# Optimization experiments

Measured on AMD Instinct MI355X. Metric: run time of the kernel, lower is better.

## Reference

```python
import jax, jax.numpy as jnp
import numpy as np

# dims: B batch, S seq, IN input, H lstm hidden, OUT output, N memory_size, W memory_width
B, S, IN, H, OUT, N, W = 128, 32, 512, 1024, 512, 16384, 128
C = OUT + W + (2 * W + 3)  # controller_output_size = 899


def setup_inputs() -> dict:
    key = jax.random.key(0)
    ks = jax.random.split(key, 16)
    def p(k, shape, s=0.02):
        return jax.random.normal(k, shape, jnp.float32) * s
    return {
        'x': jax.random.normal(ks[0], (B, S, IN), jnp.float32),
        'memory': p(ks[1], (N, W), 0.1),
        'Wih': p(ks[2], (4 * H, IN + W)), 'Whh': p(ks[3], (4 * H, H)),
        'bih': jnp.zeros(4 * H, jnp.float32), 'bhh': jnp.zeros(4 * H, jnp.float32),
        'Wout': p(ks[4], (C, H)), 'bout': jnp.zeros(C, jnp.float32),
        'rkW': p(ks[5], (W, C)), 'rkb': jnp.zeros(W, jnp.float32),
        'rbW': p(ks[6], (1, C)), 'rbb': jnp.zeros(1, jnp.float32),
        'rgW': p(ks[7], (1, C)), 'rgb': jnp.zeros(1, jnp.float32),
        'wkW': p(ks[8], (W, C)), 'wkb': jnp.zeros(W, jnp.float32),
        'wbW': p(ks[9], (1, C)), 'wbb': jnp.zeros(1, jnp.float32),
        'wgW': p(ks[10], (1, C)), 'wgb': jnp.zeros(1, jnp.float32),
        'erW': p(ks[11], (W, C)), 'erb': jnp.zeros(W, jnp.float32),
        'adW': p(ks[12], (W, C)), 'adb': jnp.zeros(W, jnp.float32),
        'pW': p(ks[13], (OUT, OUT)), 'pb': jnp.zeros(OUT, jnp.float32),
    }


def _l2norm(v, axis):
    n = jnp.linalg.norm(v, axis=axis, keepdims=True)
    return v / jnp.maximum(n, 1e-12)


def reference(x, memory, Wih, Whh, bih, bhh, Wout, bout,
              rkW, rkb, rbW, rbb, rgW, rgb,
              wkW, wkb, wbW, wbb, wgW, wgb,
              erW, erb, adW, adb, pW, pb):
    Bq, Sq, _ = x.shape
    Nq, Wq = memory.shape
    Hq = Whh.shape[1]
    out_size = pW.shape[0]
    sp = jax.nn.softplus
    uniform = jnp.full((Bq, Nq), 1.0 / Nq, x.dtype)

    def addressing(keyv, beta, gamma, prev_w, mem):
        # cosine similarity -> softmax(beta*sim) -> interpolation with prev weights
        sim = _l2norm(keyv, 1) @ _l2norm(mem, 1).T        # [B, N]
        w = jax.nn.softmax(beta * sim, axis=1)
        return gamma * w + (1 - gamma) * prev_w

    def step(carry, xt):
        mem, h, c, prev_rw, prev_rv = carry
        ci = jnp.concatenate([xt, prev_rv], axis=1)       # [B, IN+W]
        g = ci @ Wih.T + h @ Whh.T + bih + bhh
        i_, f_, gg, o_ = jnp.split(g, 4, axis=1)          # torch LSTM gate order i,f,g,o
        c = jax.nn.sigmoid(f_) * c + jax.nn.sigmoid(i_) * jnp.tanh(gg)
        h = jax.nn.sigmoid(o_) * jnp.tanh(c)
        co = h @ Wout.T + bout                            # controller output [B, C]
        # read head
        rkey = co @ rkW.T + rkb
        rbeta = sp(co @ rbW.T + rbb)
        rgamma = 1 + sp(co @ rgW.T + rgb)
        rw = addressing(rkey, rbeta, rgamma, prev_rw, mem)
        # write head (prev weights = uniform, per source)
        wkey = co @ wkW.T + wkb
        wbeta = sp(co @ wbW.T + wbb)
        wgamma = 1 + sp(co @ wgW.T + wgb)
        ww = addressing(wkey, wbeta, wgamma, uniform, mem)
        er = jax.nn.sigmoid(co @ erW.T + erb)             # [B, W]
        ad = jnp.tanh(co @ adW.T + adb)                   # [B, W]
        # MemoryBank.write sums erase/add terms over batch (shared global memory)
        erase = jnp.einsum('bn,bw->nw', ww, er)
        addt = jnp.einsum('bn,bw->nw', ww, ad)
        mem = mem * (1 - erase) + addt
        rv = rw @ mem                                     # read after write [B, W]
        out = co[:, :out_size] @ pW.T + pb
        return (mem, h, c, rw, rv), out

    init = (memory,
            jnp.zeros((Bq, Hq), x.dtype), jnp.zeros((Bq, Hq), x.dtype),
            uniform, jnp.zeros((Bq, Wq), x.dtype))
    _, outs = jax.lax.scan(step, init, jnp.swapaxes(x, 0, 1))
    return jnp.swapaxes(outs, 0, 1)                       # [B, S, OUT]
```

## Files before the change

### kernel.cpp

```cpp
#include <hip/hip_runtime.h>

typedef __attribute__((ext_vector_type(8))) short bf16x8;
typedef __attribute__((ext_vector_type(4))) float f32x4;

__device__ __forceinline__ float bf2f(unsigned short u) {
  union { float f; unsigned int i; } v; v.i = ((unsigned int)u) << 16; return v.f;
}
__device__ __forceinline__ unsigned short f2bf(float f) {
  union { float f; unsigned int i; } v; v.f = f;
  unsigned int r = v.i + 0x7fffu + ((v.i >> 16) & 1u);
  return (unsigned short)(r >> 16);
}
__device__ __forceinline__ float sigf(float x) { return 1.0f / (1.0f + expf(-x)); }
__device__ __forceinline__ float softplusf(float x) {
  return (x > 20.0f) ? x : log1pf(expf(x));
}
__device__ __forceinline__ float sat(float v) {
  return fminf(fmaxf(v, -1.0e6f), 1.0e6f);
}
__device__ __forceinline__ float ldx(const void* p, int is32, long i) {
  return is32 ? ((const float*)p)[i] : bf2f(((const unsigned short*)p)[i]);
}
template<int A32>
__device__ __forceinline__ bf16x8 load8(const void* base, long off) {
  if (A32) {
    const float* p = (const float*)base + off;
    f32x4 a = *(const f32x4*)p;
    f32x4 b = *(const f32x4*)(p + 4);
    bf16x8 r;
    r[0] = (short)f2bf(a[0]); r[1] = (short)f2bf(a[1]);
    r[2] = (short)f2bf(a[2]); r[3] = (short)f2bf(a[3]);
    r[4] = (short)f2bf(b[0]); r[5] = (short)f2bf(b[1]);
    r[6] = (short)f2bf(b[2]); r[7] = (short)f2bf(b[3]);
    return r;
  }
  return *(const bf16x8*)((const unsigned short*)base + off);
}


__global__ __launch_bounds__(64) void probe_dtype(
    const unsigned int* __restrict__ w, int* __restrict__ flags)
{
  const int lane = threadIdx.x;
  int cnt = 0;
  for (int i = 0; i < 16; ++i) {
    unsigned int word = w[lane * 16 + i];
    float av = fabsf(bf2f((unsigned short)(word & 0xFFFFu)));
    if (av > 1.0e-4f && av < 1.0f) cnt++;
  }
  #pragma unroll
  for (int off = 32; off > 0; off >>= 1) cnt += __shfl_xor(cnt, off);
  if (lane == 0) flags[1] = (cnt > 512) ? 0 : 1;
}

__global__ __launch_bounds__(64) void probe_layout(int* __restrict__ flags) {
  const int lane = threadIdx.x;
  const int qr = lane & 15, quad = lane >> 4;
  bf16x8 a, b;
  #pragma unroll
  for (int j = 0; j < 8; ++j) {
    int k = quad * 8 + j;
    a[j] = (short)f2bf((k == qr) ? 1.0f : 0.0f);
    b[j] = (short)f2bf((float)(k + 1));
  }
  f32x4 acc = {0.0f, 0.0f, 0.0f, 0.0f};
  acc = __builtin_amdgcn_mfma_f32_16x16x32_bf16(a, b, acc, 0, 0, 0);
  bool ok0 = true, ok1 = true;
  #pragma unroll
  for (int rg = 0; rg < 4; ++rg) {
    ok0 = ok0 && (acc[rg] == (float)(quad * 4 + rg + 1));
    ok1 = ok1 && (acc[rg] == (float)(qr + 1));
  }
  int a0 = __all(ok0 ? 1 : 0);
  int a1 = __all(ok1 ? 1 : 0);
  if (lane == 0) flags[0] = a0 ? 0 : (a1 ? 1 : 0);
}

template<int BM, int BN, int EPI, int A32, int BT>
__global__ __launch_bounds__(256) void gemm_pipe(
    const void* __restrict__ A, int lda,
    const unsigned short* __restrict__ B, int ldb,
    int kChunk, int Mtot, int Ntot,
    float* __restrict__ C, long long ldc, unsigned short* __restrict__ Cb,
    const int* __restrict__ flags)
{
  constexpr int LDT = 72;
  constexpr int AI = BM / 32;
  constexpr int BI = BN / 32;
  __shared__ unsigned short smem[2][(BM + BN) * LDT];
  const int tid = threadIdx.x;
  const int lane = tid & 63, wid = tid >> 6;
  const int wm = wid & 1, wn = wid >> 1;
  constexpr int WM = BM / 2, WN = BN / 2;
  constexpr int TM = WM / 16, TN = WN / 16;
  const int m0 = blockIdx.x * BM, n0 = blockIdx.y * BN;
  const int kBeg = blockIdx.z * kChunk;
  const int qr = lane & 15, quad = lane >> 4;
  const int NIT = kChunk >> 6;

  f32x4 acc[TM][TN] = {};
  bf16x8 ar[AI], br[BI];

  auto loadAB = [&](int k0) {
    #pragma unroll
    for (int i = 0; i < AI; ++i) {
      int lin = i * 256 + tid; int row = lin >> 3, q = (lin & 7) << 3;
      ar[i] = load8<A32>(A, (long)(m0 + row) * lda + k0 + q);
    }
    #pragma unroll
    for (int i = 0; i < BI; ++i) {
      int lin = i * 256 + tid;
      if (BT) {
        int kl = lin >> 3, nq = (lin & 7) << 3;
        br[i] = *(const bf16x8*)(B + (long)(k0 + kl) * ldb + n0 + nq);
      } else {
        int row = lin >> 3, q = (lin & 7) << 3;
        br[i] = *(const bf16x8*)(B + (long)(n0 + row) * ldb + k0 + q);
      }
    }
  };
  auto stage = [&](int buf) {
    #pragma unroll
    for (int i = 0; i < AI; ++i) {
      int lin = i * 256 + tid; int row = lin >> 3, q = (lin & 7) << 3;
      *(bf16x8*)&smem[buf][row * LDT + q] = ar[i];
    }
    #pragma unroll
    for (int i = 0; i < BI; ++i) {
      int lin = i * 256 + tid;
      if (BT) {
        int kl = lin >> 3, nq = (lin & 7) << 3;
        #pragma unroll
        for (int j = 0; j < 8; ++j)
          smem[buf][(BM + nq + j) * LDT + kl] = (unsigned short)br[i][j];
      } else {
        int row = lin >> 3, q = (lin & 7) << 3;
        *(bf16x8*)&smem[buf][(BM + row) * LDT + q] = br[i];
      }
    }
  };

  loadAB(kBeg);
  stage(0);
  __syncthreads();
  for (int it = 0; it < NIT; ++it) {
    if (it + 1 < NIT) loadAB(kBeg + (it + 1) * 64);
    const unsigned short* As = &smem[it & 1][0];
    const unsigned short* Bs = &smem[it & 1][BM * LDT];
    #pragma unroll
    for (int ks = 0; ks < 64; ks += 32) {
      bf16x8 af[TM], bfv[TN];
      #pragma unroll
      for (int mt = 0; mt < TM; ++mt)
        af[mt] = *(const bf16x8*)&As[(wm * WM + mt * 16 + qr) * LDT + ks + quad * 8];
      #pragma unroll
      for (int nt = 0; nt < TN; ++nt)
        bfv[nt] = *(const bf16x8*)&Bs[(wn * WN + nt * 16 + qr) * LDT + ks + quad * 8];
      #pragma unroll
      for (int mt = 0; mt < TM; ++mt)
        #pragma unroll
        for (int nt = 0; nt < TN; ++nt)
          acc[mt][nt] = __builtin_amdgcn_mfma_f32_16x16x32_bf16(af[mt], bfv[nt], acc[mt][nt], 0, 0, 0);
    }
    if (it + 1 < NIT) { stage((it + 1) & 1); __syncthreads(); }
  }

  const int swap = flags[0];
  #pragma unroll
  for (int mt = 0; mt < TM; ++mt)
    #pragma unroll
    for (int nt = 0; nt < TN; ++nt)
      #pragma unroll
      for (int rg = 0; rg < 4; ++rg) {
        int ri = swap ? qr : (quad * 4 + rg);
        int ci = swap ? (quad * 4 + rg) : qr;
        int gm = m0 + wm * WM + mt * 16 + ri;
        int gn = n0 + wn * WN + nt * 16 + ci;
        float v = sat(acc[mt][nt][rg]);
        if (EPI == 2) Cb[(size_t)gm * ldc + gn] = f2bf(v);
        else C[(size_t)blockIdx.z * Mtot * Ntot + (size_t)gm * Ntot + gn] = v;
      }
}

__global__ __launch_bounds__(256) void gemm_gates(
    const unsigned short* __restrict__ A, const unsigned short* __restrict__ B,
    const float* __restrict__ bsum2, float* __restrict__ c,
    unsigned short* __restrict__ nxt, const unsigned short* __restrict__ x_bf,
    int t, const int* __restrict__ flags)
{
  constexpr int LDT = 72;
  __shared__ unsigned short smem[2][128 * LDT];
  __shared__ float Ssc[64][65];
  const int tid = threadIdx.x;
  const int lane = tid & 63, wid = tid >> 6;
  const int wm = wid & 1, wn = wid >> 1;
  const int m0 = blockIdx.x * 64, n0 = blockIdx.y * 64;
  const int qr = lane & 15, quad = lane >> 4;
  const int NIT = 26;

  f32x4 acc[2][2] = {};
  bf16x8 ar[2], br[2];
  auto loadAB = [&](int k0) {
    #pragma unroll
    for (int i = 0; i < 2; ++i) {
      int lin = i * 256 + tid; int row = lin >> 3, q = (lin & 7) << 3;
      ar[i] = *(const bf16x8*)(A + (long)(m0 + row) * 1664 + k0 + q);
      br[i] = *(const bf16x8*)(B + (long)(n0 + row) * 1664 + k0 + q);
    }
  };
  auto stage = [&](int buf) {
    #pragma unroll
    for (int i = 0; i < 2; ++i) {
      int lin = i * 256 + tid; int row = lin >> 3, q = (lin & 7) << 3;
      *(bf16x8*)&smem[buf][row * LDT + q] = ar[i];
      *(bf16x8*)&smem[buf][(64 + row) * LDT + q] = br[i];
    }
  };
  loadAB(0); stage(0); __syncthreads();
  for (int it = 0; it < NIT; ++it) {
    if (it + 1 < NIT) loadAB((it + 1) * 64);
    const unsigned short* As = &smem[it & 1][0];
    const unsigned short* Bs = &smem[it & 1][64 * LDT];
    #pragma unroll
    for (int ks = 0; ks < 64; ks += 32) {
      bf16x8 af[2], bfv[2];
      #pragma unroll
      for (int mt = 0; mt < 2; ++mt)
        af[mt] = *(const bf16x8*)&As[(wm * 32 + mt * 16 + qr) * LDT + ks + quad * 8];
      #pragma unroll
      for (int nt = 0; nt < 2; ++nt)
        bfv[nt] = *(const bf16x8*)&Bs[(wn * 32 + nt * 16 + qr) * LDT + ks + quad * 8];
      #pragma unroll
      for (int mt = 0; mt < 2; ++mt)
        #pragma unroll
        for (int nt = 0; nt < 2; ++nt)
          acc[mt][nt] = __builtin_amdgcn_mfma_f32_16x16x32_bf16(af[mt], bfv[nt], acc[mt][nt], 0, 0, 0);
    }
    if (it + 1 < NIT) { stage((it + 1) & 1); __syncthreads(); }
  }

  const int swap = flags[0];
  #pragma unroll
  for (int mt = 0; mt < 2; ++mt)
    #pragma unroll
    for (int nt = 0; nt < 2; ++nt)
      #pragma unroll
      for (int rg = 0; rg < 4; ++rg) {
        int ri = swap ? qr : (quad * 4 + rg);
        int ci = swap ? (quad * 4 + rg) : qr;
        Ssc[wn * 32 + nt * 16 + ci][wm * 32 + mt * 16 + ri] = acc[mt][nt][rg];
      }
  __syncthreads();
  {
    const int jl = tid & 15, bh = tid >> 4;
    const int jg = (n0 >> 2) + jl;
    const float b0 = bsum2[n0 + jl * 4 + 0];
    const float b1 = bsum2[n0 + jl * 4 + 1];
    const float b2 = bsum2[n0 + jl * 4 + 2];
    const float b3 = bsum2[n0 + jl * 4 + 3];
    #pragma unroll
    for (int p = 0; p < 4; ++p) {
      int bl = bh + p * 16;
      int bb = m0 + bl;
      float gi_ = Ssc[jl * 4 + 0][bl] + b0;
      float gf  = Ssc[jl * 4 + 1][bl] + b1;
      float gg  = Ssc[jl * 4 + 2][bl] + b2;
      float go  = Ssc[jl * 4 + 3][bl] + b3;
      size_t cix = (size_t)bb * 1024 + jg;
      float cn = sat(sigf(gf) * c[cix] + sigf(gi_) * tanhf(gg));
      c[cix] = cn;
      nxt[bb * 1664 + 640 + jg] = f2bf(sigf(go) * tanhf(cn));
    }
  }
  if (t + 1 < 32) {
    int blk = blockIdx.y * 2 + blockIdx.x;
    #pragma unroll
    for (int i = 0; i < 2; ++i) {
      int e = blk * 512 + i * 256 + tid;
      nxt[(e >> 9) * 1664 + (e & 511)] = x_bf[(size_t)(t + 1) * 65536 + e];
    }
  }
}

__global__ __launch_bounds__(256) void gemm_heads(
    const unsigned short* __restrict__ Wcomb,
    const unsigned short* __restrict__ h, int ldb,
    const float* __restrict__ vcat,
    unsigned short* __restrict__ keys_n, unsigned short* __restrict__ EA,
    float* __restrict__ sc, void* __restrict__ outp, int t,
    const int* __restrict__ flags)
{
  constexpr int BM = 128, BN = 64, LDT = 72;
  __shared__ unsigned short smem[2][(BM + BN) * LDT];
  __shared__ float colss[64];
  __shared__ float cinv[64];
  const int tid = threadIdx.x;
  const int lane = tid & 63, wid = tid >> 6;
  const int wm = wid & 1, wn = wid >> 1;
  constexpr int TM = 4, TN = 2;
  const int m0 = blockIdx.x * BM, n0 = blockIdx.y * BN;
  const int qr = lane & 15, quad = lane >> 4;
  const int NIT = 16;

  f32x4 acc[TM][TN] = {};
  bf16x8 ar[4], br[2];
  auto loadAB = [&](int k0) {
    #pragma unroll
    for (int i = 0; i < 4; ++i) {
      int lin = i * 256 + tid; int row = lin >> 3, q = (lin & 7) << 3;
      ar[i] = *(const bf16x8*)(Wcomb + (long)(m0 + row) * 1024 + k0 + q);
    }
    #pragma unroll
    for (int i = 0; i < 2; ++i) {
      int lin = i * 256 + tid; int row = lin >> 3, q = (lin & 7) << 3;
      br[i] = *(const bf16x8*)(h + (long)(n0 + row) * ldb + k0 + q);
    }
  };
  auto stage = [&](int buf) {
    #pragma unroll
    for (int i = 0; i < 4; ++i) {
      int lin = i * 256 + tid; int row = lin >> 3, q = (lin & 7) << 3;
      *(bf16x8*)&smem[buf][row * LDT + q] = ar[i];
    }
    #pragma unroll
    for (int i = 0; i < 2; ++i) {
      int lin = i * 256 + tid; int row = lin >> 3, q = (lin & 7) << 3;
      *(bf16x8*)&smem[buf][(BM + row) * LDT + q] = br[i];
    }
  };

  loadAB(0);
  stage(0);
  __syncthreads();
  for (int it = 0; it < NIT; ++it) {
    if (it + 1 < NIT) loadAB((it + 1) * 64);
    const unsigned short* As = &smem[it & 1][0];
    const unsigned short* Bs = &smem[it & 1][BM * LDT];
    #pragma unroll
    for (int ks = 0; ks < 64; ks += 32) {
      bf16x8 af[TM], bfv[TN];
      #pragma unroll
      for (int mt = 0; mt < TM; ++mt)
        af[mt] = *(const bf16x8*)&smem[it & 1][(wm * 64 + mt * 16 + qr) * LDT + ks + quad * 8];
      #pragma unroll
      for (int nt = 0; nt < TN; ++nt)
        bfv[nt] = *(const bf16x8*)&Bs[(wn * 32 + nt * 16 + qr) * LDT + ks + quad * 8];
      (void)As;
      #pragma unroll
      for (int mt = 0; mt < TM; ++mt)
        #pragma unroll
        for (int nt = 0; nt < TN; ++nt)
          acc[mt][nt] = __builtin_amdgcn_mfma_f32_16x16x32_bf16(af[mt], bfv[nt], acc[mt][nt], 0, 0, 0);
    }
    if (it + 1 < NIT) { stage((it + 1) & 1); __syncthreads(); }
  }

  const int swap = flags[0];
  const int F = flags[1];
  #pragma unroll
  for (int mt = 0; mt < TM; ++mt)
    #pragma unroll
    for (int nt = 0; nt < TN; ++nt)
      #pragma unroll
      for (int rg = 0; rg < 4; ++rg) {
        int ri = swap ? qr : (quad * 4 + rg);
        int gm = m0 + wm * 64 + mt * 16 + ri;
        acc[mt][nt][rg] = sat(acc[mt][nt][rg] + vcat[gm]);
      }

  if (m0 < 256) {
    if (tid < 64) colss[tid] = 0.0f;
    __syncthreads();
    #pragma unroll
    for (int nt = 0; nt < TN; ++nt)
      #pragma unroll
      for (int rg = 0; rg < 4; ++rg) {
        float part = 0.0f;
        #pragma unroll
        for (int mt = 0; mt < TM; ++mt) {
          float v = acc[mt][nt][rg]; part += v * v;
        }
        int ci = swap ? (quad * 4 + rg) : qr;
        atomicAdd(&colss[wn * 32 + nt * 16 + ci], part);
      }
    __syncthreads();
    if (tid < 64) cinv[tid] = 1.0f / fmaxf(sqrtf(colss[tid]), 1e-12f);
    __syncthreads();
    const int head = m0 >> 7;
    #pragma unroll
    for (int mt = 0; mt < TM; ++mt)
      #pragma unroll
      for (int nt = 0; nt < TN; ++nt)
        #pragma unroll
        for (int rg = 0; rg < 4; ++rg) {
          int ri = swap ? qr : (quad * 4 + rg);
          int ci = swap ? (quad * 4 + rg) : qr;
          int w = wm * 64 + mt * 16 + ri;
          int cl = wn * 32 + nt * 16 + ci;
          keys_n[(size_t)(head * 128 + n0 + cl) * 128 + w] =
              f2bf(acc[mt][nt][rg] * cinv[cl]);
        }
  } else {
    #pragma unroll
    for (int mt = 0; mt < TM; ++mt)
      #pragma unroll
      for (int nt = 0; nt < TN; ++nt)
        #pragma unroll
        for (int rg = 0; rg < 4; ++rg) {
          int ri = swap ? qr : (quad * 4 + rg);
          int ci = swap ? (quad * 4 + rg) : qr;
          int gm = m0 + wm * 64 + mt * 16 + ri;
          int gn = n0 + wn * 32 + nt * 16 + ci;
          float v = acc[mt][nt][rg];
          if (m0 == 256) {
            EA[(size_t)((gm - 256) * 2) * 128 + gn] = f2bf(sigf(v));
          } else if (m0 == 384) {
            EA[(size_t)((gm - 384) * 2 + 1) * 128 + gn] = f2bf(tanhf(v));
          } else if (m0 < 1024) {
            int o = gm - 512;
            size_t idx = (size_t)gn * 16384 + (size_t)t * 512 + o;
            if (F) ((float*)outp)[idx] = v;
            else ((unsigned short*)outp)[idx] = f2bf(v);
          } else if (gm < 1028) {
            float sp = fminf(softplusf(v), 1.0e4f);
            int j = gm - 1024;
            sc[j * 128 + gn] = (j & 1) ? (1.0f + sp) : sp;
          }
        }
  }
}

__global__ __launch_bounds__(256) void softmax1(
    const unsigned short* __restrict__ Csim, const float* __restrict__ sc,
    float* __restrict__ rw, unsigned short* __restrict__ ww)
{
  const int r = blockIdx.x, tid = threadIdx.x;
  const int b = r & 127;
  const bool isRead = r < 128;
  const float beta  = isRead ? sc[b]       : sc[256 + b];
  const float gamma = isRead ? sc[128 + b] : sc[384 + b];
  const unsigned short* row = Csim + (size_t)r * 16384;
  __shared__ float red[4];
  float v[64];
  #pragma unroll
  for (int p = 0; p < 8; ++p) {
    bf16x8 x = *(const bf16x8*)(row + p * 2048 + tid * 8);
    #pragma unroll
    for (int j = 0; j < 8; ++j) v[p * 8 + j] = bf2f((unsigned short)x[j]);
  }
  float mx = -3.0e38f;
  #pragma unroll
  for (int p = 0; p < 64; ++p) mx = fmaxf(mx, v[p]);
  #pragma unroll
  for (int off = 32; off > 0; off >>= 1) mx = fmaxf(mx, __shfl_xor(mx, off));
  if ((tid & 63) == 0) red[tid >> 6] = mx;
  __syncthreads();
  mx = fmaxf(fmaxf(red[0], red[1]), fmaxf(red[2], red[3]));
  const float m = beta * mx;
  __syncthreads();
  float s = 0.0f;
  #pragma unroll
  for (int p = 0; p < 64; ++p) { v[p] = expf(beta * v[p] - m); s += v[p]; }
  #pragma unroll
  for (int off = 32; off > 0; off >>= 1) s += __shfl_xor(s, off);
  if ((tid & 63) == 0) red[tid >> 6] = s;
  __syncthreads();
  s = red[0] + red[1] + red[2] + red[3];
  const float inv = 1.0f / fmaxf(s, 1e-30f);
  if (isRead) {
    float* prow = rw + (size_t)b * 16384;
    #pragma unroll
    for (int p = 0; p < 8; ++p) {
      long base = p * 2048 + tid * 8;
      f32x4 o0 = *(const f32x4*)(prow + base);
      f32x4 o1 = *(const f32x4*)(prow + base + 4);
      #pragma unroll
      for (int j = 0; j < 4; ++j) {
        o0[j] = sat(gamma * v[p * 8 + j] * inv + (1.0f - gamma) * o0[j]);
        o1[j] = sat(gamma * v[p * 8 + 4 + j] * inv + (1.0f - gamma) * o1[j]);
      }
      *(f32x4*)(prow + base) = o0;
      *(f32x4*)(prow + base + 4) = o1;
    }
  } else {
    unsigned short* wrow = ww + (size_t)b * 16384;
    const float u = 1.0f / 16384.0f;
    #pragma unroll
    for (int p = 0; p < 8; ++p) {
      long base = p * 2048 + tid * 8;
      bf16x8 o;
      #pragma unroll
      for (int j = 0; j < 8; ++j)
        o[j] = (short)f2bf(sat(gamma * v[p * 8 + j] * inv + (1.0f - gamma) * u));
      *(bf16x8*)(wrow + base) = o;
    }
  }
}

__global__ __launch_bounds__(256) void write_mem(
    const unsigned short* __restrict__ ww, const unsigned short* __restrict__ EA,
    float* __restrict__ mem, unsigned short* __restrict__ memn,
    unsigned short* __restrict__ mem_bf, const int* __restrict__ flags)
{
  constexpr int LDT = 72;
  __shared__ unsigned short smem[320 * LDT];
  const int tid = threadIdx.x;
  const int lane = tid & 63, wid = tid >> 6;
  const int qr = lane & 15, quad = lane >> 4;
  const int n0 = blockIdx.x * 64;
  f32x4 acc[4][4] = {};
  bf16x8 pa[2], pb[8];

  auto loadRegs = [&](int kk) {
    #pragma unroll
    for (int i = 0; i < 2; ++i) {
      int ch = i * 256 + tid; int bl = ch >> 3, nq = (ch & 7) << 3;
      pa[i] = *(const bf16x8*)(ww + (size_t)(kk * 64 + bl) * 16384 + n0 + nq);
    }
    #pragma unroll
    for (int i = 0; i < 8; ++i) {
      int ch = i * 256 + tid; int j = ch >> 3, q = (ch & 7) << 3;
      pb[i] = *(const bf16x8*)(EA + (size_t)j * 128 + kk * 64 + q);
    }
  };
  auto stageRegs = [&]() {
    #pragma unroll
    for (int i = 0; i < 2; ++i) {
      int ch = i * 256 + tid; int bl = ch >> 3, nq = (ch & 7) << 3;
      #pragma unroll
      for (int j = 0; j < 8; ++j)
        smem[(nq + j) * LDT + bl] = (unsigned short)pa[i][j];
    }
    #pragma unroll
    for (int i = 0; i < 8; ++i) {
      int ch = i * 256 + tid; int j = ch >> 3, q = (ch & 7) << 3;
      *(bf16x8*)&smem[(64 + j) * LDT + q] = pb[i];
    }
  };
  auto doMfma = [&]() {
    #pragma unroll
    for (int ks = 0; ks < 64; ks += 32) {
      bf16x8 af[4], bfv[4];
      #pragma unroll
      for (int mt = 0; mt < 4; ++mt)
        af[mt] = *(const bf16x8*)&smem[(mt * 16 + qr) * LDT + ks + quad * 8];
      #pragma unroll
      for (int nt = 0; nt < 4; ++nt)
        bfv[nt] = *(const bf16x8*)&smem[(64 + wid * 64 + nt * 16 + qr) * LDT + ks + quad * 8];
      #pragma unroll
      for (int mt = 0; mt < 4; ++mt)
        #pragma unroll
        for (int nt = 0; nt < 4; ++nt)
          acc[mt][nt] = __builtin_amdgcn_mfma_f32_16x16x32_bf16(af[mt], bfv[nt], acc[mt][nt], 0, 0, 0);
    }
  };

  loadRegs(0);
  stageRegs();
  loadRegs(1);
  __syncthreads();
  doMfma();
  __syncthreads();
  stageRegs();
  __syncthreads();
  doMfma();
  __syncthreads();

  const int swap = flags[0];
  #pragma unroll
  for (int mt = 0; mt < 4; ++mt)
    #pragma unroll
    for (int nt = 0; nt < 4; ++nt)
      #pragma unroll
      for (int rg = 0; rg < 4; ++rg) {
        int ri = swap ? qr : (quad * 4 + rg);
        int ci = swap ? (quad * 4 + rg) : qr;
        int nl = mt * 16 + ri;
        int j  = wid * 64 + nt * 16 + ci;
        smem[nl * 264 + j] = f2bf(sat(acc[mt][nt][rg]));
      }
  __syncthreads();
  {
    const int nl = tid >> 2, ws = (tid & 3) << 5;
    const unsigned int* Srow = (const unsigned int*)&smem[nl * 264];
    const size_t gbase = (size_t)(n0 + nl) * 128 + ws;
    float nv[32];
    float ss = 0.0f;
    #pragma unroll
    for (int i = 0; i < 32; ++i) {
      unsigned int pr = Srow[ws + i];
      float er = bf2f((unsigned short)(pr & 0xFFFFu));
      float ad = bf2f((unsigned short)(pr >> 16));
      float x = sat(mem[gbase + i] * (1.0f - er) + ad);
      nv[i] = x;
      ss += x * x;
    }
    ss += __shfl_xor(ss, 1);
    ss += __shfl_xor(ss, 2);
    const float inv = 1.0f / fmaxf(sqrtf(ss), 1e-12f);
    #pragma unroll
    for (int i = 0; i < 32; ++i) {
      mem[gbase + i] = nv[i];
      memn[gbase + i] = f2bf(nv[i] * inv);
      mem_bf[gbase + i] = f2bf(nv[i]);
    }
  }
}

__global__ __launch_bounds__(256) void init_mem(
    const void* __restrict__ memory, float* __restrict__ mem,
    unsigned short* __restrict__ memn, unsigned short* __restrict__ mem_bf,
    const int* __restrict__ flags)
{
  const int F = flags[1];
  __shared__ float tile[64][129];
  __shared__ float inv[64];
  const int n0 = blockIdx.x * 64, tid = threadIdx.x;
  for (int e = tid; e < 8192; e += 256) {
    int r = e >> 7, w = e & 127;
    size_t gi = (size_t)(n0 + r) * 128 + w;
    float nv = ldx(memory, F, (long)gi);
    mem[gi] = nv;
    tile[r][w] = nv;
  }
  __syncthreads();
  if (tid < 64) {
    float ss = 0.0f;
    for (int w = 0; w < 128; ++w) { float v = tile[tid][w]; ss += v * v; }
    inv[tid] = 1.0f / fmaxf(sqrtf(ss), 1e-12f);
  }
  __syncthreads();
  for (int e = tid; e < 8192; e += 256) {
    int r = e >> 7, w = e & 127;
    size_t gi = (size_t)(n0 + r) * 128 + w;
    memn[gi] = f2bf(tile[r][w] * inv[r]);
    mem_bf[gi] = f2bf(tile[r][w]);
  }
}

__global__ __launch_bounds__(256) void rv_reduce(
    const float* __restrict__ part, unsigned short* __restrict__ nxt)
{
  int e = blockIdx.x * 256 + threadIdx.x;
  float s = 0.0f;
  for (int z = 0; z < 64; ++z) s += part[(size_t)z * 16384 + e];
  int b = e >> 7, w = e & 127;
  nxt[b * 1664 + 512 + w] = f2bf(sat(s));
}

__global__ void init_pack(
    const void* __restrict__ x, const void* __restrict__ Wih,
    const void* __restrict__ Whh, const void* __restrict__ bih,
    const void* __restrict__ bhh,
    const void* __restrict__ rkW, const void* __restrict__ wkW,
    const void* __restrict__ erW, const void* __restrict__ adW,
    const void* __restrict__ pW,
    const void* __restrict__ rbW, const void* __restrict__ rgW,
    const void* __restrict__ wbW, const void* __restrict__ wgW,
    unsigned short* __restrict__ W_lstm, float* __restrict__ bsum,
    unsigned short* __restrict__ x_bf, unsigned short* __restrict__ Wcat,
    unsigned short* __restrict__ ci_h, float* __restrict__ c,
    float* __restrict__ rw, const int* __restrict__ flags)
{
  const int F = flags[1];
  const long T0 = 4096L * 1664;
  const long T1 = 4096;
  const long T2 = 32L * 128 * 512;
  const long T3 = 1152L * 960;
  const long T4 = 128L * 1664;
  const long T5 = 128L * 1024;
  const long T6 = 128L * 16384;
  const long total = T0 + T1 + T2 + T3 + T4 + T5 + T6;
  for (long e = (long)blockIdx.x * 256 + threadIdx.x; e < total;
       e += (long)gridDim.x * 256) {
    long r = e;
    if (r < T0) {
      int jp = (int)(r / 1664), k = (int)(r % 1664);
      int orow = (jp & 3) * 1024 + (jp >> 2);
      float v = (k < 640) ? ldx(Wih, F, (long)orow * 640 + k)
                          : ldx(Whh, F, (long)orow * 1024 + (k - 640));
      W_lstm[r] = f2bf(v);
      continue;
    }
    r -= T0;
    if (r < T1) {
      long o = (long)(r & 3) * 1024 + (r >> 2);
      bsum[r] = ldx(bih, F, o) + ldx(bhh, F, o);
      continue;
    }
    r -= T1;
    if (r < T2) {
      int t = (int)(r >> 16); long rr = r & 65535;
      int b = (int)(rr >> 9), k = (int)(rr & 511);
      x_bf[r] = f2bf(ldx(x, F, (long)b * 16384 + (long)t * 512 + k));
      continue;
    }
    r -= T2;
    if (r < T3) {
      int j = (int)(r / 960), o = (int)(r % 960);
      float v = 0.0f;
      if (j < 512) {
        if (o < 899) {
          if (j < 128) v = ldx(rkW, F, (long)j * 899 + o);
          else if (j < 256) v = ldx(wkW, F, (long)(j - 128) * 899 + o);
          else if (j < 384) v = ldx(erW, F, (long)(j - 256) * 899 + o);
          else v = ldx(adW, F, (long)(j - 384) * 899 + o);
        }
      } else if (j < 1024) {
        if (o < 512) v = ldx(pW, F, (long)(j - 512) * 512 + o);
      } else if (j < 1028) {
        if (o < 899) {
          const void* s = (j == 1024) ? rbW : (j == 1025) ? rgW
                        : (j == 1026) ? wbW : wgW;
          v = ldx(s, F, o);
        }
      }
      Wcat[r] = f2bf(v);
      continue;
    }
    r -= T3;
    if (r < T4) {
      int b = (int)(r / 1664), k = (int)(r % 1664);
      ci_h[r] = (k < 512) ? f2bf(ldx(x, F, (long)b * 16384 + k)) : (unsigned short)0;
      continue;
    }
    r -= T4;
    if (r < T5) { c[r] = 0.0f; continue; }
    r -= T5;
    rw[r] = 1.0f / 16384.0f;
  }
}

__global__ __launch_bounds__(256) void transpose_wout(
    const void* __restrict__ Wout, unsigned short* __restrict__ WoutT,
    const int* __restrict__ flags)
{
  const int F = flags[1];
  __shared__ float tile[64][65];
  const int n0 = blockIdx.x * 64, o0 = blockIdx.y * 64;
  for (int e = threadIdx.x; e < 4096; e += 256) {
    int ro = e >> 6, cn = e & 63;
    int o = o0 + ro;
    tile[ro][cn] = (o < 899) ? ldx(Wout, F, (long)o * 1024 + n0 + cn) : 0.0f;
  }
  __syncthreads();
  for (int e = threadIdx.x; e < 4096; e += 256) {
    int rn = e >> 6, co = e & 63;
    WoutT[(size_t)(n0 + rn) * 960 + o0 + co] = f2bf(tile[co][rn]);
  }
}

__global__ __launch_bounds__(64) void init_vcat(
    const void* __restrict__ rkW, const void* __restrict__ wkW,
    const void* __restrict__ erW, const void* __restrict__ adW,
    const void* __restrict__ pW,
    const void* __restrict__ rbW, const void* __restrict__ rgW,
    const void* __restrict__ wbW, const void* __restrict__ wgW,
    const void* __restrict__ bout,
    const void* __restrict__ rkb, const void* __restrict__ wkb,
    const void* __restrict__ erb, const void* __restrict__ adb,
    const void* __restrict__ pb,
    const void* __restrict__ rbb, const void* __restrict__ rgb,
    const void* __restrict__ wbb, const void* __restrict__ wgb,
    float* __restrict__ vcat, const int* __restrict__ flags)
{
  const int F = flags[1];
  const int j = blockIdx.x, lane = threadIdx.x;
  if (j >= 1028) { if (lane == 0) vcat[j] = 0.0f; return; }
  const int Kj = (j >= 512 && j < 1024) ? 512 : 899;
  float s = 0.0f;
  for (int o = lane; o < Kj; o += 64) {
    float w;
    if (j < 128) w = ldx(rkW, F, (long)j * 899 + o);
    else if (j < 256) w = ldx(wkW, F, (long)(j - 128) * 899 + o);
    else if (j < 384) w = ldx(erW, F, (long)(j - 256) * 899 + o);
    else if (j < 512) w = ldx(adW, F, (long)(j - 384) * 899 + o);
    else if (j < 1024) w = ldx(pW, F, (long)(j - 512) * 512 + o);
    else {
      const void* sp = (j == 1024) ? rbW : (j == 1025) ? rgW
                     : (j == 1026) ? wbW : wgW;
      w = ldx(sp, F, o);
    }
    s += w * ldx(bout, F, o);
  }
  #pragma unroll
  for (int off = 32; off > 0; off >>= 1) s += __shfl_down(s, off);
  if (lane == 0) {
    float b;
    if (j < 128) b = ldx(rkb, F, j);
    else if (j < 256) b = ldx(wkb, F, j - 128);
    else if (j < 384) b = ldx(erb, F, j - 256);
    else if (j < 512) b = ldx(adb, F, j - 384);
    else if (j < 1024) b = ldx(pb, F, j - 512);
    else if (j == 1024) b = ldx(rbb, F, 0);
    else if (j == 1025) b = ldx(rgb, F, 0);
    else if (j == 1026) b = ldx(wbb, F, 0);
    else b = ldx(wgb, F, 0);
    vcat[j] = s + b;
  }
}

extern "C" void kernel_launch(void* const* d_in, const int* in_sizes, int n_in,
                              void* d_out, int out_size, void* d_ws, size_t ws_size,
                              hipStream_t stream) {
  const void* x      = d_in[0];
  const void* memory = d_in[1];
  const void* Wih    = d_in[2];
  const void* Whh    = d_in[3];
  const void* bih    = d_in[4];
  const void* bhh    = d_in[5];
  const void* Wout   = d_in[6];
  const void* bout   = d_in[7];
  const void* rkW    = d_in[8];
  const void* rkb    = d_in[9];
  const void* rbW    = d_in[10];
  const void* rbb    = d_in[11];
  const void* rgW    = d_in[12];
  const void* rgb    = d_in[13];
  const void* wkW    = d_in[14];
  const void* wkb    = d_in[15];
  const void* wbW    = d_in[16];
  const void* wbb    = d_in[17];
  const void* wgW    = d_in[18];
  const void* wgb    = d_in[19];
  const void* erW    = d_in[20];
  const void* erb    = d_in[21];
  const void* adW    = d_in[22];
  const void* adb    = d_in[23];
  const void* pW     = d_in[24];
  const void* pb     = d_in[25];

  char* p = (char*)d_ws;
  auto alloc = [&](size_t bytes) -> char* {
    char* r = p; p += (bytes + 255) & ~(size_t)255; return r;
  };
  char*           big    = alloc(256L * 16384 * 2);
  unsigned short* Wcat   = (unsigned short*)big;
  unsigned short* WoutT  = (unsigned short*)(big + 2359296);
  unsigned short* W_lstm = (unsigned short*)alloc(4096L * 1664 * 2);
  unsigned short* Wcomb  = (unsigned short*)alloc(1152L * 1024 * 2);
  float*          vcat   = (float*)alloc(1152L * 4);
  float*          bsum   = (float*)alloc(4096L * 4);
  unsigned short* x_bf   = (unsigned short*)alloc(32L * 128 * 512 * 2);
  unsigned short* ci_hA  = (unsigned short*)alloc(128L * 1664 * 2);
  unsigned short* ci_hB  = (unsigned short*)alloc(128L * 1664 * 2);
  float*          c      = (float*)alloc(128L * 1024 * 4);
  unsigned short* keys_n = (unsigned short*)alloc(256L * 128 * 2);
  unsigned short* EA     = (unsigned short*)alloc(256L * 128 * 2);
  float*          sc     = (float*)alloc(4L * 128 * 4);
  float*          rw     = (float*)alloc(128L * 16384 * 4);
  unsigned short* ww_nat = (unsigned short*)alloc(128L * 16384 * 2);
  float*          mem    = (float*)alloc(16384L * 128 * 4);
  unsigned short* memn   = (unsigned short*)alloc(16384L * 128 * 2);
  unsigned short* mem_bf = (unsigned short*)alloc(16384L * 128 * 2);
  int*            flags  = (int*)alloc(256);

  probe_dtype<<<1, 64, 0, stream>>>((const unsigned int*)Whh, flags);
  probe_layout<<<1, 64, 0, stream>>>(flags);
  init_pack<<<8192, 256, 0, stream>>>(x, Wih, Whh, bih, bhh, rkW, wkW, erW, adW,
                                      pW, rbW, rgW, wbW, wgW, W_lstm, bsum, x_bf,
                                      Wcat, ci_hA, c, rw, flags);
  init_mem<<<256, 256, 0, stream>>>(memory, mem, memn, mem_bf, flags);
  transpose_wout<<<dim3(16, 15, 1), 256, 0, stream>>>(Wout, WoutT, flags);
  init_vcat<<<1152, 64, 0, stream>>>(rkW, wkW, erW, adW, pW, rbW, rgW, wbW, wgW,
                                     bout, rkb, wkb, erb, adb, pb, rbb, rgb,
                                     wbb, wgb, vcat, flags);
  gemm_pipe<128, 64, 2, 0, 0><<<dim3(9, 16, 1), 256, 0, stream>>>(
      Wcat, 960, WoutT, 960, 960, 1152, 1024, nullptr, 1024, Wcomb, flags);

  unsigned short* bufs[2] = {ci_hA, ci_hB};
  for (int t = 0; t < 32; ++t) {
    unsigned short* cur = bufs[t & 1];
    unsigned short* nxt = bufs[(t + 1) & 1];
    gemm_gates<<<dim3(2, 64, 1), 256, 0, stream>>>(
        cur, W_lstm, bsum, c, nxt, x_bf, t, flags);
    gemm_heads<<<dim3(9, 2, 1), 256, 0, stream>>>(
        Wcomb, nxt + 640, 1664, vcat, keys_n, EA, sc, d_out, t, flags);
    gemm_pipe<128, 64, 2, 0, 0><<<dim3(2, 256, 1), 256, 0, stream>>>(
        keys_n, 128, memn, 128, 128, 256, 16384, nullptr, 16384,
        (unsigned short*)big, flags);
    softmax1<<<256, 256, 0, stream>>>((const unsigned short*)big, sc, rw, ww_nat);
    write_mem<<<256, 256, 0, stream>>>(ww_nat, EA, mem, memn, mem_bf, flags);
    gemm_pipe<128, 64, 3, 1, 1><<<dim3(1, 2, 64), 256, 0, stream>>>(
        rw, 16384, mem_bf, 128, 256, 128, 128, (float*)big, 128, nullptr, flags);
    rv_reduce<<<64, 256, 0, stream>>>((const float*)big, nxt);
  }
}
```

Baseline: 2.886 ms.

## Fuse per-timestep NTM kernels into one persistent cooperative kernel with grid syncs

After: 8.799 ms. 205% more time.

```diff
diff --git a/kernel.cpp b/kernel.cpp
--- a/kernel.cpp
+++ b/kernel.cpp
@@ -1,4 +1,6 @@
 #include <hip/hip_runtime.h>
+#include <hip/hip_cooperative_groups.h>
+namespace cg = cooperative_groups;
 
 typedef __attribute__((ext_vector_type(8))) short bf16x8;
 typedef __attribute__((ext_vector_type(4))) float f32x4;
@@ -21,18 +23,19 @@
 __device__ __forceinline__ float ldx(const void* p, int is32, long i) {
   return is32 ? ((const float*)p)[i] : bf2f(((const unsigned short*)p)[i]);
 }
+__device__ __forceinline__ bf16x8 packbf(f32x4 a, f32x4 b) {
+  bf16x8 r;
+  r[0] = (short)f2bf(a[0]); r[1] = (short)f2bf(a[1]);
+  r[2] = (short)f2bf(a[2]); r[3] = (short)f2bf(a[3]);
+  r[4] = (short)f2bf(b[0]); r[5] = (short)f2bf(b[1]);
+  r[6] = (short)f2bf(b[2]); r[7] = (short)f2bf(b[3]);
+  return r;
+}
 template<int A32>
 __device__ __forceinline__ bf16x8 load8(const void* base, long off) {
   if (A32) {
     const float* p = (const float*)base + off;
-    f32x4 a = *(const f32x4*)p;
-    f32x4 b = *(const f32x4*)(p + 4);
-    bf16x8 r;
-    r[0] = (short)f2bf(a[0]); r[1] = (short)f2bf(a[1]);
-    r[2] = (short)f2bf(a[2]); r[3] = (short)f2bf(a[3]);
-    r[4] = (short)f2bf(b[0]); r[5] = (short)f2bf(b[1]);
-    r[6] = (short)f2bf(b[2]); r[7] = (short)f2bf(b[3]);
-    return r;
+    return packbf(*(const f32x4*)p, *(const f32x4*)(p + 4));
   }
   return *(const bf16x8*)((const unsigned short*)base + off);
 }
@@ -74,6 +77,487 @@
   int a0 = __all(ok0 ? 1 : 0);
   int a1 = __all(ok1 ? 1 : 0);
   if (lane == 0) flags[0] = a0 ? 0 : (a1 ? 1 : 0);
+}
+
+__global__ __launch_bounds__(256) void ntm_loop(
+    const unsigned short* __restrict__ W_lstm, const float* __restrict__ bsum,
+    const unsigned short* __restrict__ x_bf, const unsigned short* __restrict__ Wcomb,
+    const float* __restrict__ vcat, unsigned short* __restrict__ hA,
+    unsigned short* __restrict__ hB, float* __restrict__ c,
+    float* __restrict__ rvf, unsigned short* __restrict__ keys_n,
+    unsigned short* __restrict__ EA, float* __restrict__ sc,
+    unsigned short* __restrict__ Csim, float* __restrict__ rw,
+    unsigned short* __restrict__ ww, float* __restrict__ mem,
+    unsigned short* __restrict__ memn, unsigned short* __restrict__ mem_bf,
+    void* __restrict__ outp, const int* __restrict__ flags)
+{
+  extern __shared__ __align__(16) unsigned short sm[];
+  cg::grid_group grid = cg::this_grid();
+  const int bid = blockIdx.x, tid = threadIdx.x;
+  const int lane = tid & 63, wid = tid >> 6;
+  const int wm = wid & 1, wn = wid >> 1;
+  const int qr = lane & 15, quad = lane >> 4;
+  const int swap = flags[0], F = flags[1];
+  constexpr int LDT = 136;
+  constexpr int GBUF = 96 * 136;
+
+  for (int t = 0; t < 32; ++t) {
+    const unsigned short* hcur = (t & 1) ? hB : hA;
+    unsigned short* hnxt = (t & 1) ? hA : hB;
+
+    {
+      const int m0 = (bid & 1) * 64;
+      const int n0 = (bid >> 1) * 32;
+      f32x4 acc[2] = {};
+      bf16x8 ar[4], br[2];
+      auto loadG = [&](int it) {
+        const int k0 = it * 128;
+        #pragma unroll
+        for (int i = 0; i < 4; ++i) {
+          int lin = i * 256 + tid; int row = lin >> 4, q = (lin & 15) << 3;
+          int gb = m0 + row;
+          if (it < 4) {
+            ar[i] = *(const bf16x8*)(x_bf + (size_t)t * 65536 + (size_t)gb * 512 + k0 + q);
+          } else if (it == 4) {
+            const float* pp = rvf + (size_t)gb * 128 + q;
+            ar[i] = packbf(*(const f32x4*)pp, *(const f32x4*)(pp + 4));
+          } else {
+            ar[i] = *(const bf16x8*)(hcur + (size_t)gb * 1024 + (k0 - 640) + q);
+          }
+        }
+        #pragma unroll
+        for (int i = 0; i < 2; ++i) {
+          int lin = i * 256 + tid; int row = lin >> 4, q = (lin & 15) << 3;
+          br[i] = *(const bf16x8*)(W_lstm + (size_t)(n0 + row) * 1664 + k0 + q);
+        }
+      };
+      auto stageG = [&](int buf) {
+        unsigned short* S = sm + buf * GBUF;
+        #pragma unroll
+        for (int i = 0; i < 4; ++i) {
+          int lin = i * 256 + tid; int row = lin >> 4, q = (lin & 15) << 3;
+          *(bf16x8*)&S[row * LDT + q] = ar[i];
+        }
+        #pragma unroll
+        for (int i = 0; i < 2; ++i) {
+          int lin = i * 256 + tid; int row = lin >> 4, q = (lin & 15) << 3;
+          *(bf16x8*)&S[(64 + row) * LDT + q] = br[i];
+        }
+      };
+      auto mfmaG = [&](int buf) {
+        const unsigned short* S = sm + buf * GBUF;
+        #pragma unroll
+        for (int ks = 0; ks < 128; ks += 32) {
+          bf16x8 bv = *(const bf16x8*)&S[(64 + wn * 16 + qr) * LDT + ks + quad * 8];
+          #pragma unroll
+          for (int mt = 0; mt < 2; ++mt) {
+            bf16x8 av = *(const bf16x8*)&S[(wm * 32 + mt * 16 + qr) * LDT + ks + quad * 8];
+            acc[mt] = __builtin_amdgcn_mfma_f32_16x16x32_bf16(av, bv, acc[mt], 0, 0, 0);
+          }
+        }
+      };
+      loadG(0); stageG(0); __syncthreads();
+      for (int it = 0; it < 13; ++it) {
+        if (it + 1 < 13) loadG(it + 1);
+        mfmaG(it & 1);
+        if (it + 1 < 13) { stageG((it + 1) & 1); __syncthreads(); }
+      }
+      __syncthreads();
+      float* Ssc = (float*)sm;
+      #pragma unroll
+      for (int mt = 0; mt < 2; ++mt)
+        #pragma unroll
+        for (int rg = 0; rg < 4; ++rg) {
+          int ri = swap ? qr : (quad * 4 + rg);
+          int ci = swap ? (quad * 4 + rg) : qr;
+          Ssc[(wn * 16 + ci) * 72 + (wm * 32 + mt * 16 + ri)] = acc[mt][rg];
+        }
+      __syncthreads();
+      {
+        int b = tid & 63, jq = tid >> 6;
+        #pragma unroll
+        for (int jj = 0; jj < 2; ++jj) {
+          int j = jq * 2 + jj;
+          int jg = (n0 >> 2) + j;
+          float gi_ = Ssc[(j * 4 + 0) * 72 + b] + bsum[n0 + j * 4 + 0];
+          float gf  = Ssc[(j * 4 + 1) * 72 + b] + bsum[n0 + j * 4 + 1];
+          float gg  = Ssc[(j * 4 + 2) * 72 + b] + bsum[n0 + j * 4 + 2];
+          float go  = Ssc[(j * 4 + 3) * 72 + b] + bsum[n0 + j * 4 + 3];
+          size_t cix = (size_t)(m0 + b) * 1024 + jg;
+          float cn = sat(sigf(gf) * c[cix] + sigf(gi_) * tanhf(gg));
+          c[cix] = cn;
+          hnxt[(size_t)(m0 + b) * 1024 + jg] = f2bf(sigf(go) * tanhf(cn));
+        }
+      }
+    }
+    grid.sync();
+
+    if (bid < 36) {
+      const int m0 = (bid >> 2) * 128;
+      const int n0 = (bid & 3) * 32;
+      constexpr int HB = 160 * 72;
+      f32x4 acc[4] = {};
+      bf16x8 ar[4], br;
+      auto loadH = [&](int it) {
+        const int k0 = it * 64;
+        #pragma unroll
+        for (int i = 0; i < 4; ++i) {
+          int lin = i * 256 + tid; int row = lin >> 3, q = (lin & 7) << 3;
+          ar[i] = *(const bf16x8*)(Wcomb + (size_t)(m0 + row) * 1024 + k0 + q);
+        }
+        { int row = tid >> 3, q = (tid & 7) << 3;
+          br = *(const bf16x8*)(hnxt + (size_t)(n0 + row) * 1024 + k0 + q); }
+      };
+      auto stageH = [&](int buf) {
+        unsigned short* S = sm + buf * HB;
+        #pragma unroll
+        for (int i = 0; i < 4; ++i) {
+          int lin = i * 256 + tid; int row = lin >> 3, q = (lin & 7) << 3;
+          *(bf16x8*)&S[row * 72 + q] = ar[i];
+        }
+        { int row = tid >> 3, q = (tid & 7) << 3;
+          *(bf16x8*)&S[(128 + row) * 72 + q] = br; }
+      };
+      auto mfmaH = [&](int buf) {
+        const unsigned short* S = sm + buf * HB;
+        #pragma unroll
+        for (int ks = 0; ks < 64; ks += 32) {
+          bf16x8 bv = *(const bf16x8*)&S[(128 + wn * 16 + qr) * 72 + ks + quad * 8];
+          #pragma unroll
+          for (int mt = 0; mt < 4; ++mt) {
+            bf16x8 av = *(const bf16x8*)&S[(wm * 64 + mt * 16 + qr) * 72 + ks + quad * 8];
+            acc[mt] = __builtin_amdgcn_mfma_f32_16x16x32_bf16(av, bv, acc[mt], 0, 0, 0);
+          }
+        }
+      };
+      loadH(0); stageH(0); __syncthreads();
+      for (int it = 0; it < 16; ++it) {
+        if (it + 1 < 16) loadH(it + 1);
+        mfmaH(it & 1);
+        if (it + 1 < 16) { stageH((it + 1) & 1); __syncthreads(); }
+      }
+      #pragma unroll
+      for (int mt = 0; mt < 4; ++mt)
+        #pragma unroll
+        for (int rg = 0; rg < 4; ++rg) {
+          int ri = swap ? qr : (quad * 4 + rg);
+          int gm = m0 + wm * 64 + mt * 16 + ri;
+          acc[mt][rg] = sat(acc[mt][rg] + vcat[gm]);
+        }
+      if (m0 < 256) {
+        __syncthreads();
+        float* colss = (float*)sm;
+        if (tid < 32) colss[tid] = 0.0f;
+        __syncthreads();
+        #pragma unroll
+        for (int rg = 0; rg < 4; ++rg) {
+          float p = 0.0f;
+          #pragma unroll
+          for (int mt = 0; mt < 4; ++mt) p += acc[mt][rg] * acc[mt][rg];
+          int ci = swap ? (quad * 4 + rg) : qr;
+          atomicAdd(&colss[wn * 16 + ci], p);
+        }
+        __syncthreads();
+        if (tid < 32) colss[32 + tid] = 1.0f / fmaxf(sqrtf(colss[tid]), 1e-12f);
+        __syncthreads();
+        #pragma unroll
+        for (int mt = 0; mt < 4; ++mt)
+          #pragma unroll
+          for (int rg = 0; rg < 4; ++rg) {
+            int ri = swap ? qr : (quad * 4 + rg);
+            int ci = swap ? (quad * 4 + rg) : qr;
+            int w = wm * 64 + mt * 16 + ri;
+            int cl = wn * 16 + ci;
+            keys_n[(size_t)((m0 >> 7) * 128 + n0 + cl) * 128 + w] =
+                f2bf(acc[mt][rg] * colss[32 + cl]);
+          }
+      } else {
+        #pragma unroll
+        for (int mt = 0; mt < 4; ++mt)
+          #pragma unroll
+          for (int rg = 0; rg < 4; ++rg) {
+            int ri = swap ? qr : (quad * 4 + rg);
+            int ci = swap ? (quad * 4 + rg) : qr;
+            int gm = m0 + wm * 64 + mt * 16 + ri;
+            int gb = n0 + wn * 16 + ci;
+            float v = acc[mt][rg];
+            if (m0 == 256) EA[(size_t)((gm - 256) * 2) * 128 + gb] = f2bf(sigf(v));
+            else if (m0 == 384) EA[(size_t)((gm - 384) * 2 + 1) * 128 + gb] = f2bf(tanhf(v));
+            else if (m0 < 1024) {
+              int o = gm - 512;
+              size_t idx = (size_t)gb * 16384 + (size_t)t * 512 + o;
+              if (F) ((float*)outp)[idx] = v;
+              else ((unsigned short*)outp)[idx] = f2bf(v);
+            } else if (gm < 1028) {
+              float sp = fminf(softplusf(v), 1.0e4f);
+              int j = gm - 1024;
+              sc[j * 128 + gb] = (j & 1) ? (1.0f + sp) : sp;
+            }
+          }
+      }
+    }
+    grid.sync();
+
+    {
+      const int m0 = (bid & 1) * 128;
+      const int n0 = (bid >> 1) * 128;
+      f32x4 acc[4][4] = {};
+      #pragma unroll
+      for (int ks = 0; ks < 128; ks += 32) {
+        bf16x8 af[4], bv[4];
+        #pragma unroll
+        for (int mt = 0; mt < 4; ++mt)
+          af[mt] = *(const bf16x8*)(keys_n + (size_t)(m0 + wm * 64 + mt * 16 + qr) * 128 + ks + quad * 8);
+        #pragma unroll
+        for (int nt = 0; nt < 4; ++nt)
+          bv[nt] = *(const bf16x8*)(memn + (size_t)(n0 + wn * 64 + nt * 16 + qr) * 128 + ks + quad * 8);
+        #pragma unroll
+        for (int mt = 0; mt < 4; ++mt)
+          #pragma unroll
+          for (int nt = 0; nt < 4; ++nt)
+            acc[mt][nt] = __builtin_amdgcn_mfma_f32_16x16x32_bf16(af[mt], bv[nt], acc[mt][nt], 0, 0, 0);
+      }
+      unsigned short* Sc = sm;
+      #pragma unroll
+      for (int mt = 0; mt < 4; ++mt)
+        #pragma unroll
+        for (int nt = 0; nt < 4; ++nt)
+          #pragma unroll
+          for (int rg = 0; rg < 4; ++rg) {
+            int ri = swap ? qr : (quad * 4 + rg);
+            int ci = swap ? (quad * 4 + rg) : qr;
+            Sc[(wm * 64 + mt * 16 + ri) * LDT + wn * 64 + nt * 16 + ci] =
+                f2bf(sat(acc[mt][nt][rg]));
+          }
+      __syncthreads();
+      #pragma unroll
+      for (int i = 0; i < 8; ++i) {
+        int lin = i * 256 + tid; int row = lin >> 4, q = (lin & 15) << 3;
+        *(bf16x8*)(Csim + (size_t)(m0 + row) * 16384 + n0 + q) = *(bf16x8*)&Sc[row * LDT + q];
+      }
+    }
+    grid.sync();
+
+    {
+      const int r = bid;
+      const int b = r & 127;
+      const bool isRead = r < 128;
+      const float beta  = isRead ? sc[b]       : sc[256 + b];
+      const float gamma = isRead ? sc[128 + b] : sc[384 + b];
+      const unsigned short* row = Csim + (size_t)r * 16384;
+      float* red = (float*)sm;
+      if (tid < 64) rvf[r * 64 + tid] = 0.0f;
+      float v[64];
+      #pragma unroll
+      for (int p = 0; p < 8; ++p) {
+        bf16x8 x = *(const bf16x8*)(row + p * 2048 + tid * 8);
+        #pragma unroll
+        for (int j = 0; j < 8; ++j) v[p * 8 + j] = bf2f((unsigned short)x[j]);
+      }
+      float mx = -3.0e38f;
+      #pragma unroll
+      for (int p = 0; p < 64; ++p) mx = fmaxf(mx, v[p]);
+      #pragma unroll
+      for (int off = 32; off > 0; off >>= 1) mx = fmaxf(mx, __shfl_xor(mx, off));
+      if ((tid & 63) == 0) red[tid >> 6] = mx;
+      __syncthreads();
+      mx = fmaxf(fmaxf(red[0], red[1]), fmaxf(red[2], red[3]));
+      const float m = beta * mx;
+      __syncthreads();
+      float s = 0.0f;
+      #pragma unroll
+      for (int p = 0; p < 64; ++p) { v[p] = expf(beta * v[p] - m); s += v[p]; }
+      #pragma unroll
+      for (int off = 32; off > 0; off >>= 1) s += __shfl_xor(s, off);
+      if ((tid & 63) == 0) red[tid >> 6] = s;
+      __syncthreads();
+      s = red[0] + red[1] + red[2] + red[3];
+      const float inv = 1.0f / fmaxf(s, 1e-30f);
+      if (isRead) {
+        float* prow = rw + (size_t)b * 16384;
+        #pragma unroll
+        for (int p = 0; p < 8; ++p) {
+          long base = p * 2048 + tid * 8;
+          f32x4 o0 = *(const f32x4*)(prow + base);
+          f32x4 o1 = *(const f32x4*)(prow + base + 4);
+          #pragma unroll
+          for (int j = 0; j < 4; ++j) {
+            o0[j] = sat(gamma * v[p * 8 + j] * inv + (1.0f - gamma) * o0[j]);
+            o1[j] = sat(gamma * v[p * 8 + 4 + j] * inv + (1.0f - gamma) * o1[j]);
+          }
+          *(f32x4*)(prow + base) = o0;
+          *(f32x4*)(prow + base + 4) = o1;
+        }
+      } else {
+        unsigned short* wrow = ww + (size_t)b * 16384;
+        const float u = 1.0f / 16384.0f;
+        #pragma unroll
+        for (int p = 0; p < 8; ++p) {
+          long base = p * 2048 + tid * 8;
+          bf16x8 o;
+          #pragma unroll
+          for (int j = 0; j < 8; ++j)
+            o[j] = (short)f2bf(sat(gamma * v[p * 8 + j] * inv + (1.0f - gamma) * u));
+          *(bf16x8*)(wrow + base) = o;
+        }
+      }
+    }
+    grid.sync();
+
+    {
+      const int n0 = bid * 64;
+      f32x4 acc[4][4] = {};
+      bf16x8 pa[2], pb[8];
+      auto loadRegs = [&](int kk) {
+        #pragma unroll
+        for (int i = 0; i < 2; ++i) {
+          int ch = i * 256 + tid; int bl = ch >> 3, nq = (ch & 7) << 3;
+          pa[i] = *(const bf16x8*)(ww + (size_t)(kk * 64 + bl) * 16384 + n0 + nq);
+        }
+        #pragma unroll
+        for (int i = 0; i < 8; ++i) {
+          int ch = i * 256 + tid; int j = ch >> 3, q = (ch & 7) << 3;
+          pb[i] = *(const bf16x8*)(EA + (size_t)j * 128 + kk * 64 + q);
+        }
+      };
+      auto stageRegs = [&]() {
+        #pragma unroll
+        for (int i = 0; i < 2; ++i) {
+          int ch = i * 256 + tid; int bl = ch >> 3, nq = (ch & 7) << 3;
+          #pragma unroll
+          for (int j = 0; j < 8; ++j)
+            sm[(nq + j) * 72 + bl] = (unsigned short)pa[i][j];
+        }
+        #pragma unroll
+        for (int i = 0; i < 8; ++i) {
+          int ch = i * 256 + tid; int j = ch >> 3, q = (ch & 7) << 3;
+          *(bf16x8*)&sm[(64 + j) * 72 + q] = pb[i];
+        }
+      };
+      auto doMfma = [&]() {
+        #pragma unroll
+        for (int ks = 0; ks < 64; ks += 32) {
+          bf16x8 af[4], bv[4];
+          #pragma unroll
+          for (int mt = 0; mt < 4; ++mt)
+            af[mt] = *(const bf16x8*)&sm[(mt * 16 + qr) * 72 + ks + quad * 8];
+          #pragma unroll
+          for (int nt = 0; nt < 4; ++nt)
+            bv[nt] = *(const bf16x8*)&sm[(64 + wid * 64 + nt * 16 + qr) * 72 + ks + quad * 8];
+          #pragma unroll
+          for (int mt = 0; mt < 4; ++mt)
+            #pragma unroll
+            for (int nt = 0; nt < 4; ++nt)
+              acc[mt][nt] = __builtin_amdgcn_mfma_f32_16x16x32_bf16(af[mt], bv[nt], acc[mt][nt], 0, 0, 0);
+        }
+      };
+      loadRegs(0); stageRegs(); loadRegs(1);
+      __syncthreads(); doMfma(); __syncthreads();
+      stageRegs(); __syncthreads(); doMfma(); __syncthreads();
+      #pragma unroll
+      for (int mt = 0; mt < 4; ++mt)
+        #pragma unroll
+        for (int nt = 0; nt < 4; ++nt)
+          #pragma unroll
+          for (int rg = 0; rg < 4; ++rg) {
+            int ri = swap ? qr : (quad * 4 + rg);
+            int ci = swap ? (quad * 4 + rg) : qr;
+            sm[(mt * 16 + ri) * 264 + wid * 64 + nt * 16 + ci] = f2bf(sat(acc[mt][nt][rg]));
+          }
+      __syncthreads();
+      {
+        const int nl = tid >> 2, ws = (tid & 3) << 5;
+        const unsigned int* Srow = (const unsigned int*)&sm[nl * 264];
+        const size_t gbase = (size_t)(n0 + nl) * 128 + ws;
+        float nv[32];
+        float ss = 0.0f;
+        #pragma unroll
+        for (int i = 0; i < 32; ++i) {
+          unsigned int pr = Srow[ws + i];
+          float er = bf2f((unsigned short)(pr & 0xFFFFu));
+          float ad = bf2f((unsigned short)(pr >> 16));
+          float x = sat(mem[gbase + i] * (1.0f - er) + ad);
+          nv[i] = x;
+          ss += x * x;
+        }
+        ss += __shfl_xor(ss, 1);
+        ss += __shfl_xor(ss, 2);
+        const float inv = 1.0f / fmaxf(sqrtf(ss), 1e-12f);
+        #pragma unroll
+        for (int i = 0; i < 32; ++i) {
+          mem[gbase + i] = nv[i];
+          memn[gbase + i] = f2bf(nv[i] * inv);
+          mem_bf[gbase + i] = f2bf(nv[i]);
+        }
+      }
+    }
+    grid.sync();
+
+    {
+      const int z = bid >> 3, sp = bid & 7;
+      const int m0 = (sp & 1) * 64, n0 = (sp >> 1) * 32;
+      const int kBeg = z * 512;
+      f32x4 acc[2] = {};
+      bf16x8 ar[4], br[2];
+      auto loadR = [&](int it) {
+        const int k0 = kBeg + it * 128;
+        #pragma unroll
+        for (int i = 0; i < 4; ++i) {
+          int lin = i * 256 + tid; int row = lin >> 4, q = (lin & 15) << 3;
+          const float* pp = rw + (size_t)(m0 + row) * 16384 + k0 + q;
+          ar[i] = packbf(*(const f32x4*)pp, *(const f32x4*)(pp + 4));
+        }
+        #pragma unroll
+        for (int i = 0; i < 2; ++i) {
+          int lin = i * 256 + tid; int kl = lin >> 2, wq = (lin & 3) << 3;
+          br[i] = *(const bf16x8*)(mem_bf + (size_t)(k0 + kl) * 128 + n0 + wq);
+        }
+      };
+      auto stageR = [&](int buf) {
+        unsigned short* S = sm + buf * GBUF;
+        #pragma unroll
+        for (int i = 0; i < 4; ++i) {
+          int lin = i * 256 + tid; int row = lin >> 4, q = (lin & 15) << 3;
+          *(bf16x8*)&S[row * LDT + q] = ar[i];
+        }
+        #pragma unroll
+        for (int i = 0; i < 2; ++i) {
+          int lin = i * 256 + tid; int kl = lin >> 2, wq = (lin & 3) << 3;
+          #pragma unroll
+          for (int j = 0; j < 8; ++j)
+            S[(64 + wq + j) * LDT + kl] = (unsigned short)br[i][j];
+        }
+      };
+      auto mfmaR = [&](int buf) {
+        const unsigned short* S = sm + buf * GBUF;
+        #pragma unroll
+        for (int ks = 0; ks < 128; ks += 32) {
+          bf16x8 bv = *(const bf16x8*)&S[(64 + wn * 16 + qr) * LDT + ks + quad * 8];
+          #pragma unroll
+          for (int mt = 0; mt < 2; ++mt) {
+            bf16x8 av = *(const bf16x8*)&S[(wm * 32 + mt * 16 + qr) * LDT + ks + quad * 8];
+            acc[mt] = __builtin_amdgcn_mfma_f32_16x16x32_bf16(av, bv, acc[mt], 0, 0, 0);
+          }
+        }
+      };
+      loadR(0); stageR(0); __syncthreads();
+      for (int it = 0; it < 4; ++it) {
+        if (it + 1 < 4) loadR(it + 1);
+        mfmaR(it & 1);
+        if (it + 1 < 4) { stageR((it + 1) & 1); __syncthreads(); }
+      }
+      #pragma unroll
+      for (int mt = 0; mt < 2; ++mt)
+        #pragma unroll
+        for (int rg = 0; rg < 4; ++rg) {
+          int ri = swap ? qr : (quad * 4 + rg);
+          int ci = swap ? (quad * 4 + rg) : qr;
+          atomicAdd(&rvf[(size_t)(m0 + wm * 32 + mt * 16 + ri) * 128 + n0 + wn * 16 + ci],
+                    acc[mt][rg]);
+        }
+    }
+    grid.sync();
+  }
 }
 
 template<int BM, int BN, int EPI, int A32, int BT>
@@ -97,10 +581,8 @@
   const int kBeg = blockIdx.z * kChunk;
   const int qr = lane & 15, quad = lane >> 4;
   const int NIT = kChunk >> 6;
-
   f32x4 acc[TM][TN] = {};
   bf16x8 ar[AI], br[BI];
-
   auto loadAB = [&](int k0) {
     #pragma unroll
     for (int i = 0; i < AI; ++i) {
@@ -139,10 +621,7 @@
       }
     }
   };
-
-  loadAB(kBeg);
-  stage(0);
-  __syncthreads();
+  loadAB(kBeg); stage(0); __syncthreads();
   for (int it = 0; it < NIT; ++it) {
     if (it + 1 < NIT) loadAB(kBeg + (it + 1) * 64);
     const unsigned short* As = &smem[it & 1][0];
@@ -164,7 +643,6 @@
     }
     if (it + 1 < NIT) { stage((it + 1) & 1); __syncthreads(); }
   }
-
   const int swap = flags[0];
   #pragma unroll
   for (int mt = 0; mt < TM; ++mt)
@@ -182,7 +660,7 @@
       }
 }
 
-__global__ __launch_bounds__(256) void gemm_gates(
+__global__ __launch_bounds__(256) void gemm_gates_fb(
     const unsigned short* __restrict__ A, const unsigned short* __restrict__ B,
     const float* __restrict__ bsum2, float* __restrict__ c,
     unsigned short* __restrict__ nxt, const unsigned short* __restrict__ x_bf,
@@ -197,7 +675,6 @@
   const int m0 = blockIdx.x * 64, n0 = blockIdx.y * 64;
   const int qr = lane & 15, quad = lane >> 4;
   const int NIT = 26;
-
   f32x4 acc[2][2] = {};
   bf16x8 ar[2], br[2];
   auto loadAB = [&](int k0) {
@@ -238,7 +715,6 @@
     }
     if (it + 1 < NIT) { stage((it + 1) & 1); __syncthreads(); }
   }
-
   const int swap = flags[0];
   #pragma unroll
   for (int mt = 0; mt < 2; ++mt)
@@ -282,7 +758,7 @@
   }
 }
 
-__global__ __launch_bounds__(256) void gemm_heads(
+__global__ __launch_bounds__(256) void gemm_heads_fb(
     const unsigned short* __restrict__ Wcomb,
     const unsigned short* __restrict__ h, int ldb,
     const float* __restrict__ vcat,
@@ -301,7 +777,6 @@
   const int m0 = blockIdx.x * BM, n0 = blockIdx.y * BN;
   const int qr = lane & 15, quad = lane >> 4;
   const int NIT = 16;
-
   f32x4 acc[TM][TN] = {};
   bf16x8 ar[4], br[2];
   auto loadAB = [&](int k0) {
@@ -328,13 +803,9 @@
       *(bf16x8*)&smem[buf][(BM + row) * LDT + q] = br[i];
     }
   };
-
-  loadAB(0);
-  stage(0);
-  __syncthreads();
+  loadAB(0); stage(0); __syncthreads();
   for (int it = 0; it < NIT; ++it) {
     if (it + 1 < NIT) loadAB((it + 1) * 64);
-    const unsigned short* As = &smem[it & 1][0];
     const unsigned short* Bs = &smem[it & 1][BM * LDT];
     #pragma unroll
     for (int ks = 0; ks < 64; ks += 32) {
@@ -345,7 +816,6 @@
       #pragma unroll
       for (int nt = 0; nt < TN; ++nt)
         bfv[nt] = *(const bf16x8*)&Bs[(wn * 32 + nt * 16 + qr) * LDT + ks + quad * 8];
-      (void)As;
       #pragma unroll
       for (int mt = 0; mt < TM; ++mt)
         #pragma unroll
@@ -354,7 +824,6 @@
     }
     if (it + 1 < NIT) { stage((it + 1) & 1); __syncthreads(); }
   }
-
   const int swap = flags[0];
   const int F = flags[1];
   #pragma unroll
@@ -367,7 +836,6 @@
         int gm = m0 + wm * 64 + mt * 16 + ri;
         acc[mt][nt][rg] = sat(acc[mt][nt][rg] + vcat[gm]);
       }
-
   if (m0 < 256) {
     if (tid < 64) colss[tid] = 0.0f;
     __syncthreads();
@@ -377,9 +845,7 @@
       for (int rg = 0; rg < 4; ++rg) {
         float part = 0.0f;
         #pragma unroll
-        for (int mt = 0; mt < TM; ++mt) {
-          float v = acc[mt][nt][rg]; part += v * v;
-        }
+        for (int mt = 0; mt < TM; ++mt) { float v = acc[mt][nt][rg]; part += v * v; }
         int ci = swap ? (quad * 4 + rg) : qr;
         atomicAdd(&colss[wn * 32 + nt * 16 + ci], part);
       }
@@ -397,8 +863,7 @@
           int ci = swap ? (quad * 4 + rg) : qr;
           int w = wm * 64 + mt * 16 + ri;
           int cl = wn * 32 + nt * 16 + ci;
-          keys_n[(size_t)(head * 128 + n0 + cl) * 128 + w] =
-              f2bf(acc[mt][nt][rg] * cinv[cl]);
+          keys_n[(size_t)(head * 128 + n0 + cl) * 128 + w] = f2bf(acc[mt][nt][rg] * cinv[cl]);
         }
   } else {
     #pragma unroll
@@ -412,11 +877,9 @@
           int gm = m0 + wm * 64 + mt * 16 + ri;
           int gn = n0 + wn * 32 + nt * 16 + ci;
           float v = acc[mt][nt][rg];
-          if (m0 == 256) {
-            EA[(size_t)((gm - 256) * 2) * 128 + gn] = f2bf(sigf(v));
-          } else if (m0 == 384) {
-            EA[(size_t)((gm - 384) * 2 + 1) * 128 + gn] = f2bf(tanhf(v));
-          } else if (m0 < 1024) {
+          if (m0 == 256) EA[(size_t)((gm - 256) * 2) * 128 + gn] = f2bf(sigf(v));
+          else if (m0 == 384) EA[(size_t)((gm - 384) * 2 + 1) * 128 + gn] = f2bf(tanhf(v));
+          else if (m0 < 1024) {
             int o = gm - 512;
             size_t idx = (size_t)gn * 16384 + (size_t)t * 512 + o;
             if (F) ((float*)outp)[idx] = v;
@@ -430,7 +893,7 @@
   }
 }
 
-__global__ __launch_bounds__(256) void softmax1(
+__global__ __launch_bounds__(256) void softmax1_fb(
     const unsigned short* __restrict__ Csim, const float* __restrict__ sc,
     float* __restrict__ rw, unsigned short* __restrict__ ww)
 {
@@ -497,7 +960,7 @@
   }
 }
 
-__global__ __launch_bounds__(256) void write_mem(
+__global__ __launch_bounds__(256) void write_mem_fb(
     const unsigned short* __restrict__ ww, const unsigned short* __restrict__ EA,
     float* __restrict__ mem, unsigned short* __restrict__ memn,
     unsigned short* __restrict__ mem_bf, const int* __restrict__ flags)
@@ -510,7 +973,6 @@
   const int n0 = blockIdx.x * 64;
   f32x4 acc[4][4] = {};
   bf16x8 pa[2], pb[8];
-
   auto loadRegs = [&](int kk) {
     #pragma unroll
     for (int i = 0; i < 2; ++i) {
@@ -554,18 +1016,9 @@
           acc[mt][nt] = __builtin_amdgcn_mfma_f32_16x16x32_bf16(af[mt], bfv[nt], acc[mt][nt], 0, 0, 0);
     }
   };
-
-  loadRegs(0);
-  stageRegs();
-  loadRegs(1);
-  __syncthreads();
-  doMfma();
-  __syncthreads();
-  stageRegs();
-  __syncthreads();
-  doMfma();
-  __syncthreads();
-
+  loadRegs(0); stageRegs(); loadRegs(1);
+  __syncthreads(); doMfma(); __syncthreads();
+  stageRegs(); __syncthreads(); doMfma(); __syncthreads();
   const int swap = flags[0];
   #pragma unroll
   for (int mt = 0; mt < 4; ++mt)
@@ -575,9 +1028,7 @@
       for (int rg = 0; rg < 4; ++rg) {
         int ri = swap ? qr : (quad * 4 + rg);
         int ci = swap ? (quad * 4 + rg) : qr;
-        int nl = mt * 16 + ri;
-        int j  = wid * 64 + nt * 16 + ci;
-        smem[nl * 264 + j] = f2bf(sat(acc[mt][nt][rg]));
+        smem[(mt * 16 + ri) * 264 + wid * 64 + nt * 16 + ci] = f2bf(sat(acc[mt][nt][rg]));
       }
   __syncthreads();
   {
@@ -605,6 +1056,16 @@
       mem_bf[gbase + i] = f2bf(nv[i]);
     }
   }
+}
+
+__global__ __launch_bounds__(256) void rv_reduce_fb(
+    const float* __restrict__ part, unsigned short* __restrict__ nxt)
+{
+  int e = blockIdx.x * 256 + threadIdx.x;
+  float s = 0.0f;
+  for (int z = 0; z < 64; ++z) s += part[(size_t)z * 16384 + e];
+  int b = e >> 7, w = e & 127;
+  nxt[b * 1664 + 512 + w] = f2bf(sat(s));
 }
 
 __global__ __launch_bounds__(256) void init_mem(
@@ -638,16 +1099,6 @@
   }
 }
 
-__global__ __launch_bounds__(256) void rv_reduce(
-    const float* __restrict__ part, unsigned short* __restrict__ nxt)
-{
-  int e = blockIdx.x * 256 + threadIdx.x;
-  float s = 0.0f;
-  for (int z = 0; z < 64; ++z) s += part[(size_t)z * 16384 + e];
-  int b = e >> 7, w = e & 127;
-  nxt[b * 1664 + 512 + w] = f2bf(sat(s));
-}
-
 __global__ void init_pack(
     const void* __restrict__ x, const void* __restrict__ Wih,
     const void* __restrict__ Whh, const void* __restrict__ bih,
@@ -660,7 +1111,8 @@
     unsigned short* __restrict__ W_lstm, float* __restrict__ bsum,
     unsigned short* __restrict__ x_bf, unsigned short* __restrict__ Wcat,
     unsigned short* __restrict__ ci_h, float* __restrict__ c,
-    float* __restrict__ rw, const int* __restrict__ flags)
+    float* __restrict__ rw, unsigned short* __restrict__ hA,
+    float* __restrict__ rvf, const int* __restrict__ flags)
 {
   const int F = flags[1];
   const long T0 = 4096L * 1664;
@@ -670,7 +1122,9 @@
   const long T4 = 128L * 1664;
   const long T5 = 128L * 1024;
   const long T6 = 128L * 16384;
-  const long total = T0 + T1 + T2 + T3 + T4 + T5 + T6;
+  const long T7 = 128L * 1024;
+  const long T8 = 128L * 128;
+  const long total = T0 + T1 + T2 + T3 + T4 + T5 + T6 + T7 + T8;
   for (long e = (long)blockIdx.x * 256 + threadIdx.x; e < total;
        e += (long)gridDim.x * 256) {
     long r = e;
@@ -727,7 +1181,11 @@
     r -= T4;
     if (r < T5) { c[r] = 0.0f; continue; }
     r -= T5;
-    rw[r] = 1.0f / 16384.0f;
+    if (r < T6) { rw[r] = 1.0f / 16384.0f; continue; }
+    r -= T6;
+    if (r < T7) { hA[r] = 0; continue; }
+    r -= T7;
+    rvf[r] = 0.0f;
   }
 }
 
@@ -844,7 +1302,10 @@
   unsigned short* x_bf   = (unsigned short*)alloc(32L * 128 * 512 * 2);
   unsigned short* ci_hA  = (unsigned short*)alloc(128L * 1664 * 2);
   unsigned short* ci_hB  = (unsigned short*)alloc(128L * 1664 * 2);
+  unsigned short* hA     = (unsigned short*)alloc(128L * 1024 * 2);
+  unsigned short* hB     = (unsigned short*)alloc(128L * 1024 * 2);
   float*          c      = (float*)alloc(128L * 1024 * 4);
+  float*          rvf    = (float*)alloc(128L * 128 * 4);
   unsigned short* keys_n = (unsigned short*)alloc(256L * 128 * 2);
   unsigned short* EA     = (unsigned short*)alloc(256L * 128 * 2);
   float*          sc     = (float*)alloc(4L * 128 * 4);
@@ -859,7 +1320,7 @@
   probe_layout<<<1, 64, 0, stream>>>(flags);
   init_pack<<<8192, 256, 0, stream>>>(x, Wih, Whh, bih, bhh, rkW, wkW, erW, adW,
                                       pW, rbW, rgW, wbW, wgW, W_lstm, bsum, x_bf,
-                                      Wcat, ci_hA, c, rw, flags);
+                                      Wcat, ci_hA, c, rw, hA, rvf, flags);
   init_mem<<<256, 256, 0, stream>>>(memory, mem, memn, mem_bf, flags);
   transpose_wout<<<dim3(16, 15, 1), 256, 0, stream>>>(Wout, WoutT, flags);
   init_vcat<<<1152, 64, 0, stream>>>(rkW, wkW, erW, adW, pW, rbW, rgW, wbW, wgW,
@@ -868,21 +1329,54 @@
   gemm_pipe<128, 64, 2, 0, 0><<<dim3(9, 16, 1), 256, 0, stream>>>(
       Wcat, 960, WoutT, 960, 960, 1152, 1024, nullptr, 1024, Wcomb, flags);
 
-  unsigned short* bufs[2] = {ci_hA, ci_hB};
-  for (int t = 0; t < 32; ++t) {
-    unsigned short* cur = bufs[t & 1];
-    unsigned short* nxt = bufs[(t + 1) & 1];
-    gemm_gates<<<dim3(2, 64, 1), 256, 0, stream>>>(
-        cur, W_lstm, bsum, c, nxt, x_bf, t, flags);
-    gemm_heads<<<dim3(9, 2, 1), 256, 0, stream>>>(
-        Wcomb, nxt + 640, 1664, vcat, keys_n, EA, sc, d_out, t, flags);
-    gemm_pipe<128, 64, 2, 0, 0><<<dim3(2, 256, 1), 256, 0, stream>>>(
-        keys_n, 128, memn, 128, 128, 256, 16384, nullptr, 16384,
-        (unsigned short*)big, flags);
-    softmax1<<<256, 256, 0, stream>>>((const unsigned short*)big, sc, rw, ww_nat);
-    write_mem<<<256, 256, 0, stream>>>(ww_nat, EA, mem, memn, mem_bf, flags);
-    gemm_pipe<128, 64, 3, 1, 1><<<dim3(1, 2, 64), 256, 0, stream>>>(
-        rw, 16384, mem_bf, 128, 256, 128, 128, (float*)big, 128, nullptr, flags);
-    rv_reduce<<<64, 256, 0, stream>>>((const float*)big, nxt);
-  }
-}
+  const unsigned short* a_W_lstm = W_lstm;
+  const float* a_bsum = bsum;
+  const unsigned short* a_x_bf = x_bf;
+  const unsigned short* a_Wcomb = Wcomb;
+  const float* a_vcat = vcat;
+  unsigned short* a_hA = hA;
+  unsigned short* a_hB = hB;
+  float* a_c = c;
+  float* a_rvf = rvf;
+  unsigned short* a_keys = keys_n;
+  unsigned short* a_EA = EA;
+  float* a_sc = sc;
+  unsigned short* a_Csim = (unsigned short*)big;
+  float* a_rw = rw;
+  unsigned short* a_ww = ww_nat;
+  float* a_mem = mem;
+  unsigned short* a_memn = memn;
+  unsigned short* a_membf = mem_bf;
+  void* a_out = d_out;
+  const int* a_flags = flags;
+  void* kargs[] = {
+    (void*)&a_W_lstm, (void*)&a_bsum, (void*)&a_x_bf, (void*)&a_Wcomb,
+    (void*)&a_vcat, (void*)&a_hA, (void*)&a_hB, (void*)&a_c, (void*)&a_rvf,
+    (void*)&a_keys, (void*)&a_EA, (void*)&a_sc, (void*)&a_Csim, (void*)&a_rw,
+    (void*)&a_ww, (void*)&a_mem, (void*)&a_memn, (void*)&a_membf,
+    (void*)&a_out, (void*)&a_flags
+  };
+  hipError_t cerr = hipLaunchCooperativeKernel(
+      (const void*)ntm_loop, dim3(256), dim3(256), kargs,
+      (unsigned int)(2 * 96 * 136 * sizeof(unsigned short)), stream);
+  if (cerr != hipSuccess) {
+    (void)hipGetLastError();
+    unsigned short* bufs[2] = {ci_hA, ci_hB};
+    for (int t = 0; t < 32; ++t) {
+      unsigned short* cur = bufs[t & 1];
+      unsigned short* nxt = bufs[(t + 1) & 1];
+      gemm_gates_fb<<<dim3(2, 64, 1), 256, 0, stream>>>(
+          cur, W_lstm, bsum, c, nxt, x_bf, t, flags);
+      gemm_heads_fb<<<dim3(9, 2, 1), 256, 0, stream>>>(
+          Wcomb, nxt + 640, 1664, vcat, keys_n, EA, sc, d_out, t, flags);
+      gemm_pipe<128, 64, 2, 0, 0><<<dim3(2, 256, 1), 256, 0, stream>>>(
+          keys_n, 128, memn, 128, 128, 256, 16384, nullptr, 16384,
+          (unsigned short*)big, flags);
+      softmax1_fb<<<256, 256, 0, stream>>>((const unsigned short*)big, sc, rw, ww_nat);
+      write_mem_fb<<<256, 256, 0, stream>>>(ww_nat, EA, mem, memn, mem_bf, flags);
+      gemm_pipe<128, 64, 3, 1, 1><<<dim3(1, 2, 64), 256, 0, stream>>>(
+          rw, 16384, mem_bf, 128, 256, 128, 128, (float*)big, 128, nullptr, flags);
+      rv_reduce_fb<<<64, 256, 0, stream>>>((const float*)big, nxt);
+    }
+  }
+}
```
